# Kernel optimization log

Measured on AMD Instinct MI355X. Metric: run time of the kernel, lower is better.

## Reference

```python
import jax, jax.numpy as jnp
import numpy as np
from jax.ops import segment_sum, segment_max

N_NODES = 100000
N_EDGES = 3200000
F_IN = 512
HIDDEN = 64
N_CLASSES = 16
N_HOPS = 2
LAMBDA_GRAPH = 0.2
LEAKY_ALPHA = 0.2


def setup_inputs() -> dict:
    key = jax.random.key(0)
    ks = jax.random.split(key, 8)
    X = jax.random.normal(ks[0], (N_NODES, F_IN), dtype=jnp.float32)
    W0 = jax.random.normal(ks[1], (F_IN, HIDDEN), dtype=jnp.float32) * (1.0 / np.sqrt(F_IN))
    W1 = jax.random.normal(ks[2], (HIDDEN, N_CLASSES), dtype=jnp.float32) * (1.0 / np.sqrt(HIDDEN))
    a1 = jax.random.normal(ks[3], (N_CLASSES, 1), dtype=jnp.float32)
    a2 = jax.random.normal(ks[4], (N_CLASSES, 1), dtype=jnp.float32)
    W_attn = jax.random.normal(ks[5], (N_NODES, N_CLASSES), dtype=jnp.float32) * 0.1
    gcn_vals = jax.random.uniform(ks[6], (N_EDGES,), dtype=jnp.float32) / 32.0
    edge_index = jax.random.randint(ks[7], (2, N_EDGES), 0, N_NODES, dtype=jnp.int32)
    return {"X": X, "W0": W0, "W1": W1, "a1": a1, "a2": a2,
            "W_attn": W_attn, "gcn_vals": gcn_vals, "edge_index": edge_index}


def _sp_attn_head(Z, src, dst, gcn_vals, a1, a2):
    # per-node scalar scores (GAT-style)
    f1 = (Z @ a1)[:, 0]  # [N]
    f2 = (Z @ a2)[:, 0]  # [N]
    e = jax.nn.leaky_relu(f1[src] + f2[dst], negative_slope=LEAKY_ALPHA)  # [E]
    # sparse softmax over each row (segment by src)
    m = segment_max(e, src, num_segments=N_NODES)
    ex = jnp.exp(e - m[src])
    s = segment_sum(ex, src, num_segments=N_NODES)
    soft = ex / s[src]
    coef = gcn_vals * (1.0 - LAMBDA_GRAPH) + soft * LAMBDA_GRAPH  # [E]
    # sparse_tensor_dense_matmul: out[i] = sum_j coef_ij * Z[j]
    vals = segment_sum(coef[:, None] * Z[dst], src, num_segments=N_NODES)  # [N,C]
    return vals


def reference(X, W0, W1, a1, a2, W_attn, gcn_vals, edge_index):
    src, dst = edge_index[0], edge_index[1]
    # dense MLP layers (inference: keep_prob = 1 => no dropout)
    H = jax.nn.relu(X @ W0)           # [N, HIDDEN]
    Z = H @ W1                        # logits_local [N, C]
    hops = [Z]
    for _ in range(N_HOPS):
        hops.append(_sp_attn_head(hops[-1], src, dst, gcn_vals, a1, a2))
    P = jnp.stack(hops, axis=1)       # [N, K, C]
    # _build_attn: per-node attention over hops
    attn = jnp.einsum('nkc,nc->nk', P, W_attn)
    ceof = jax.nn.softmax(attn, axis=1)
    out = jnp.einsum('nkc,nk->nc', P, ceof)  # [N, C]
    return out
```

## Files before the change

### kernel.cpp

```cpp
#include <hip/hip_runtime.h>
#include <hip/hip_fp16.h>

#define NN 100000
#define NE 3200000
#define FIN 512
#define HIDN 64
#define NC 16
#define LEAKY 0.2f
#define LG 0.2f

#define GM 256
#define HLD2 72
#define MLP_BLKS 391

#define BSH 9
#define NBUCK 196
#define TILE_A 4096
#define SLACK 20480

typedef float4 f4;
typedef short bf16x8 __attribute__((ext_vector_type(8)));
typedef float f32x4 __attribute__((ext_vector_type(4)));
typedef unsigned short ushort_t;

__device__ __forceinline__ bf16x8 cvt8(const f4 a, const f4 b) {
  union { unsigned u[4]; bf16x8 v; } o;
  asm("v_cvt_pk_bf16_f32 %0, %1, %2" : "=v"(o.u[0]) : "v"(a.x), "v"(a.y));
  asm("v_cvt_pk_bf16_f32 %0, %1, %2" : "=v"(o.u[1]) : "v"(a.z), "v"(a.w));
  asm("v_cvt_pk_bf16_f32 %0, %1, %2" : "=v"(o.u[2]) : "v"(b.x), "v"(b.y));
  asm("v_cvt_pk_bf16_f32 %0, %1, %2" : "=v"(o.u[3]) : "v"(b.z), "v"(b.w));
  return o.v;
}

__device__ __forceinline__ float bf16f(ushort_t s) {
  return __uint_as_float(((unsigned)s) << 16);
}
__device__ __forceinline__ ushort_t f2bf(float f) {
  const unsigned u = __float_as_uint(f);
  return (ushort_t)((u + 0x7fffu + ((u >> 16) & 1u)) >> 16);
}
__device__ __forceinline__ int2 ldnt(const int2* p) {
  const int* q = (const int*)p;
  int2 r;
  r.x = __builtin_nontemporal_load(q);
  r.y = __builtin_nontemporal_load(q + 1);
  return r;
}

__global__ __launch_bounds__(256) void k_w0t(const float* __restrict__ W0,
                                             short* __restrict__ W0T,
                                             int* __restrict__ bcnt,
                                             int* __restrict__ gcur) {
  const int i = blockIdx.x*256 + threadIdx.x;
  if (blockIdx.x == 0) {
    bcnt[threadIdx.x] = 0;
    gcur[threadIdx.x] = threadIdx.x * SLACK;
  }
  if (i >= HIDN*FIN) return;
  const int c = i >> 9, k = i & 511;
  W0T[i] = (short)f2bf(W0[(size_t)k*HIDN + c]);
}

__global__ __launch_bounds__(512, 2) void k_mlp3(
    const float* __restrict__ X, const short* __restrict__ W0T,
    const float* __restrict__ W1, const float* __restrict__ a1v,
    const float* __restrict__ a2v, float* __restrict__ Z,
    ushort_t* __restrict__ Zb, float* __restrict__ f1o, float* __restrict__ f2o)
{
  __shared__ __align__(16) char smem[HIDN*FIN*2];
  short* Wb = (short*)smem;
  short (*HsB)[HLD2] = (short(*)[HLD2])smem;
  float* W1s = (float*)(smem + GM*HLD2*2);
  const int t = threadIdx.x;
  const int wid = t >> 6, lane = t & 63;
  const int r = lane & 15, g = lane >> 4;
  const int rowbase = blockIdx.x*GM + wid*32;
  int row0 = rowbase + r;       if (row0 >= NN) row0 = NN-1;
  int row1 = rowbase + 16 + r;  if (row1 >= NN) row1 = NN-1;
  const float* pa0 = X + (size_t)row0*FIN + g*8;
  const float* pa1 = X + (size_t)row1*FIN + g*8;

  f4 xs[4][2][2];
  #pragma unroll
  for (int d=0; d<4; ++d) {
    xs[d][0][0] = *(const f4*)(pa0 + d*32);  xs[d][0][1] = *(const f4*)(pa0 + d*32 + 4);
    xs[d][1][0] = *(const f4*)(pa1 + d*32);  xs[d][1][1] = *(const f4*)(pa1 + d*32 + 4);
  }

  #pragma unroll
  for (int i2 = 0; i2 < 8; ++i2) {
    const int i = t + i2*512;
    const int row = i >> 6;
    const int cb = (i & 63) << 4;
    const bf16x8 v = *(const bf16x8*)(W0T + (size_t)row*FIN + (i & 63)*8);
    *(bf16x8*)((char*)Wb + row*1024 + (cb ^ ((row & 7) << 4))) = v;
  }
  __syncthreads();

  f32x4 acc[2][4];
  #pragma unroll
  for (int m=0;m<2;++m)
    #pragma unroll
    for (int n=0;n<4;++n) acc[m][n] = (f32x4){0.f,0.f,0.f,0.f};

  #pragma unroll
  for (int ks=0; ks<16; ++ks) {
    const int st = ks & 3;
    bf16x8 bh[4];
    #pragma unroll
    for (int n=0;n<4;++n) {
      const int wrow = n*16 + r;
      const int boff = wrow*1024 + ((ks*64 + g*16) ^ ((wrow & 7) << 4));
      bh[n] = *(const bf16x8*)((const char*)Wb + boff);
    }
    const bf16x8 xb0 = cvt8(xs[st][0][0], xs[st][0][1]);
    const bf16x8 xb1 = cvt8(xs[st][1][0], xs[st][1][1]);
    if (ks + 4 < 16) {
      const int ko = (ks+4)*32;
      xs[st][0][0] = *(const f4*)(pa0 + ko);  xs[st][0][1] = *(const f4*)(pa0 + ko + 4);
      xs[st][1][0] = *(const f4*)(pa1 + ko);  xs[st][1][1] = *(const f4*)(pa1 + ko + 4);
    }
    #pragma unroll
    for (int n=0;n<4;++n) {
      acc[0][n] = __builtin_amdgcn_mfma_f32_16x16x32_bf16(xb0, bh[n], acc[0][n], 0,0,0);
      acc[1][n] = __builtin_amdgcn_mfma_f32_16x16x32_bf16(xb1, bh[n], acc[1][n], 0,0,0);
    }
  }
  __syncthreads();

  #pragma unroll
  for (int m=0;m<2;++m) {
    const int hr = wid*32 + m*16 + g*4;
    #pragma unroll
    for (int n=0;n<4;++n)
      #pragma unroll
      for (int q=0;q<4;++q)
        HsB[hr+q][n*16+r] = (short)f2bf(fmaxf(acc[m][n][q], 0.f));
  }
  if (t < 256) *(f4*)(W1s + t*4) = *(const f4*)(W1 + t*4);
  __syncthreads();

  {
    const int en = t >> 1, half = t & 1;
    const int node = blockIdx.x*GM + en;
    if (node < NN) {
      float z[8];
      #pragma unroll
      for (int j=0;j<8;++j) z[j]=0.f;
      const bf16x8* hp = (const bf16x8*)(&HsB[en][0]);
      #pragma unroll
      for (int h8=0; h8<8; ++h8) {
        const bf16x8 hv8 = hp[h8];
        #pragma unroll
        for (int j=0;j<8;++j) {
          const float hv = bf16f((ushort_t)hv8[j]);
          const int h = h8*8 + j;
          const f4 wa = *(const f4*)(W1s + h*NC + half*8);
          const f4 wb = *(const f4*)(W1s + h*NC + half*8 + 4);
          z[0]+=hv*wa.x; z[1]+=hv*wa.y; z[2]+=hv*wa.z; z[3]+=hv*wa.w;
          z[4]+=hv*wb.x; z[5]+=hv*wb.y; z[6]+=hv*wb.z; z[7]+=hv*wb.w;
        }
      }
      f4* zp = (f4*)(Z + (size_t)node*NC + half*8);
      zp[0] = make_float4(z[0],z[1],z[2],z[3]);
      zp[1] = make_float4(z[4],z[5],z[6],z[7]);
      bf16x8 zb;
      #pragma unroll
      for (int j=0;j<8;++j) zb[j] = (short)f2bf(z[j]);
      *(bf16x8*)(Zb + (size_t)node*NC + half*8) = zb;
      float s1=0.f, s2=0.f;
      #pragma unroll
      for (int j=0;j<8;++j) { s1 += z[j]*a1v[half*8+j]; s2 += z[j]*a2v[half*8+j]; }
      s1 += __shfl_xor(s1, 1);
      s2 += __shfl_xor(s2, 1);
      if (half == 0) { f1o[node] = s1; f2o[node] = s2; }
    }
  }
}

__global__ __launch_bounds__(512) void k_binA(const int* __restrict__ src,
    const int* __restrict__ dst, const float* __restrict__ gcn,
    int* __restrict__ bcnt, int* __restrict__ gcur, int2* __restrict__ tmp)
{
  __shared__ int cnt[256];
  __shared__ int scn[256];
  __shared__ int cur[256];
  __shared__ int gbase[256];
  __shared__ int2 stage[TILE_A];
  __shared__ unsigned char sb[TILE_A];
  const int t = threadIdx.x;
  const int e0 = blockIdx.x*TILE_A;
  const int ecount = min(TILE_A, NE - e0);
  if (t < 256) cnt[t] = 0;
  __syncthreads();
  int w0v[8], w1v[8], bv[8];
  #pragma unroll
  for (int it=0; it<8; ++it) {
    const int i = e0 + it*512 + t;
    bv[it] = -1;
    if (i < NE) {
      const int s_ = src[i];
      const int b = s_ >> BSH;
      bv[it] = b;
      w0v[it] = dst[i] | ((s_ & ((1<<BSH)-1)) << 17);
      w1v[it] = __float_as_int(gcn[i]);
      atomicAdd(&cnt[b], 1);
    }
  }
  __syncthreads();
  if (t < 256) scn[t] = cnt[t];
  __syncthreads();
  for (int off=1; off<256; off<<=1) {
    const int x = (t>=off && t<256) ? scn[t-off] : 0;
    __syncthreads();
    if (t < 256) scn[t] += x;
    __syncthreads();
  }
  if (t < 256) {
    cur[t] = scn[t] - cnt[t];
    if (cnt[t] > 0) {
      gbase[t] = atomicAdd(&gcur[t], cnt[t]);
      atomicAdd(&bcnt[t], cnt[t]);
    }
  }
  __syncthreads();
  #pragma unroll
  for (int it=0; it<8; ++it) {
    if (bv[it] >= 0) {
      const int pos = atomicAdd(&cur[bv[it]], 1);
      stage[pos] = make_int2(w0v[it], w1v[it]);
      sb[pos] = (unsigned char)bv[it];
    }
  }
  __syncthreads();
  #pragma unroll
  for (int it=0; it<8; ++it) {
    const int slot = it*512 + t;
    if (slot < ecount) {
      const int b = sb[slot];
      const int gd = gbase[b] + slot - (scn[b] - cnt[b]);
      tmp[gd] = stage[slot];
    }
  }
}

__global__ __launch_bounds__(512) void k_binB(const int* __restrict__ bcnt,
    const int2* __restrict__ tmp, int* __restrict__ rowptr, int2* __restrict__ cvp)
{
  __shared__ int cnt[512];
  __shared__ int scn[512];
  __shared__ int cur[512];
  __shared__ int bs[256];
  __shared__ int baseSh;
  const int t = threadIdx.x;
  const int b = blockIdx.x;
  const int node0 = b << BSH;
  const int n = bcnt[b];
  const int2* tsl = tmp + (size_t)b*SLACK;
  if (t < 256) bs[t] = (t < NBUCK) ? bcnt[t] : 0;
  cnt[t] = 0;
  __syncthreads();
  for (int off=1; off<256; off<<=1) {
    const int x = (t>=off && t<256) ? bs[t-off] : 0;
    __syncthreads();
    if (t < 256) bs[t] += x;
    __syncthreads();
  }
  if (t == 0) baseSh = bs[b] - n;
  __syncthreads();
  const int base = baseSh;
  for (int i = t; i < n; i += 512)
    atomicAdd(&cnt[tsl[i].x >> 17], 1);
  __syncthreads();
  scn[t] = cnt[t];
  __syncthreads();
  for (int off=1; off<512; off<<=1) {
    const int x = (t>=off) ? scn[t-off] : 0;
    __syncthreads();
    scn[t] += x;
    __syncthreads();
  }
  const int excl = scn[t] - cnt[t];
  cur[t] = excl;
  if (node0 + t < NN) rowptr[node0 + t] = base + excl;
  if (b == 0 && t == 0) rowptr[NN] = NE;
  __syncthreads();
  for (int i = t; i < n; i += 512) {
    const int2 e = tsl[i];
    const int ls = e.x >> 17;
    const int p = base + atomicAdd(&cur[ls], 1);
    cvp[p] = make_int2(e.x & 0x1FFFF, e.y);
  }
}

__global__ __launch_bounds__(256) void k_hop(const int* __restrict__ rowptr,
    const int2* __restrict__ cvp,
    const ushort_t* __restrict__ Zb, const float* __restrict__ f1in,
    const float* __restrict__ f2in, ushort_t* __restrict__ Zoutb,
    float* __restrict__ f1out, float* __restrict__ f2out,
    const float* __restrict__ a1v, const float* __restrict__ a2v)
{
  __shared__ __align__(16) int2 rowbuf[8][64];
  const int t = threadIdx.x;
  const int lane = t & 31;
  const int hw = t >> 5;
  const int row = blockIdx.x*8 + hw;
  if (row >= NN) return;
  const int start = rowptr[row], end = rowptr[row+1];
  const int deg = end - start;
  const int c = lane & 15, g = (lane >> 4) & 1;

  if (deg == 0) {
    if (g == 0) {
      Zoutb[(size_t)row*NC + c] = 0;
      if (c == 0) { f1out[row] = 0.f; f2out[row] = 0.f; }
    }
    return;
  }
  const float f1r = f1in[row];

  if (deg <= 64) {
    int cc0 = 0, cc1 = 0; float vv0 = 0.f, vv1 = 0.f;
    float e0 = -1e30f, e1 = -1e30f;
    if (lane < deg) {
      const int2 p = ldnt(&cvp[start + lane]);
      cc0 = p.x; vv0 = __int_as_float(p.y);
      const float x = f1r + f2in[cc0];
      e0 = (x > 0.f) ? x : LEAKY*x;
    }
    if (32 + lane < deg) {
      const int2 p = ldnt(&cvp[start + 32 + lane]);
      cc1 = p.x; vv1 = __int_as_float(p.y);
      const float x = f1r + f2in[cc1];
      e1 = (x > 0.f) ? x : LEAKY*x;
    }
    float m = fmaxf(e0, e1);
    #pragma unroll
    for (int msk=1; msk<32; msk<<=1) m = fmaxf(m, __shfl_xor(m, msk));
    const float ex0 = (lane < deg) ? __expf(e0 - m) : 0.f;
    const float ex1 = (32 + lane < deg) ? __expf(e1 - m) : 0.f;
    float s = ex0 + ex1;
    #pragma unroll
    for (int msk=1; msk<32; msk<<=1) s += __shfl_xor(s, msk);
    const float lgs = LG / s;
    const int npass = (deg + 3) >> 2;
    if (lane < deg)
      rowbuf[hw][lane] = make_int2(cc0, __float_as_int((1.f-LG)*vv0 + ex0*lgs));
    if (32 + lane < deg)
      rowbuf[hw][32 + lane] = make_int2(cc1, __float_as_int((1.f-LG)*vv1 + ex1*lgs));
    for (int z = deg + lane; z < 4*npass; z += 32) rowbuf[hw][z] = make_int2(0, 0);
    asm volatile("s_waitcnt lgkmcnt(0)" ::: "memory");
    float accv = 0.f;
    for (int p0 = 0; p0 < npass; p0 += 8) {
      int4 pr[8]; ushort_t u0[8], u1[8];
      #pragma unroll
      for (int j=0;j<8;++j) {
        if (p0 + j < npass)
          pr[j] = *(const int4*)(&rowbuf[hw][(p0+j)*4 + g*2]);
        else
          pr[j] = make_int4(0, 0, 0, 0);
      }
      #pragma unroll
      for (int j=0;j<8;++j) {
        u0[j] = Zb[(size_t)pr[j].x*NC + c];
        u1[j] = Zb[(size_t)pr[j].z*NC + c];
      }
      #pragma unroll
      for (int j=0;j<8;++j) {
        accv += __int_as_float(pr[j].y) * bf16f(u0[j]);
        accv += __int_as_float(pr[j].w) * bf16f(u1[j]);
      }
    }
    accv += __shfl_xor(accv, 16);
    if (g == 0) {
      Zoutb[(size_t)row*NC + c] = f2bf(accv);
      float s1 = accv * a1v[c];
      float s2 = accv * a2v[c];
      #pragma unroll
      for (int msk=1; msk<16; msk<<=1) { s1 += __shfl_xor(s1, msk); s2 += __shfl_xor(s2, msk); }
      if (c == 0) { f1out[row] = s1; f2out[row] = s2; }
    }
  } else {
    const int nit = (deg + 31) >> 5;
    float m = -1e30f;
    for (int it=0; it<nit; ++it) {
      const int idx = start + it*32 + lane;
      if (idx < end) {
        const int2 p = ldnt(&cvp[idx]);
        const float x = f1r + f2in[p.x];
        m = fmaxf(m, (x>0.f)?x:LEAKY*x);
      }
    }
    #pragma unroll
    for (int msk=1; msk<32; msk<<=1) m = fmaxf(m, __shfl_xor(m, msk));
    float s = 0.f;
    for (int it=0; it<nit; ++it) {
      const int idx = start + it*32 + lane;
      if (idx < end) {
        const int2 p = ldnt(&cvp[idx]);
        const float x = f1r + f2in[p.x];
        s += __expf(((x>0.f)?x:LEAKY*x) - m);
      }
    }
    #pragma unroll
    for (int msk=1; msk<32; msk<<=1) s += __shfl_xor(s, msk);
    const float lgs = LG / s;
    float a[16];
    #pragma unroll
    for (int k=0;k<16;++k) a[k]=0.f;
    for (int it=0; it<nit; ++it) {
      const int idx = start + it*32 + lane;
      if (idx < end) {
        const int2 p = ldnt(&cvp[idx]);
        const float x = f1r + f2in[p.x];
        const float coef = (1.f-LG)*__int_as_float(p.y) + __expf(((x>0.f)?x:LEAKY*x) - m)*lgs;
        const ushort_t* zp = Zb + (size_t)p.x*NC;
        #pragma unroll
        for (int k=0;k<16;++k) a[k] += coef * bf16f(zp[k]);
      }
    }
    #pragma unroll
    for (int msk=1; msk<32; msk<<=1) {
      #pragma unroll
      for (int k=0;k<16;++k) a[k] += __shfl_xor(a[k], msk);
    }
    if (lane == 0) {
      #pragma unroll
      for (int k=0;k<16;++k) Zoutb[(size_t)row*NC + k] = f2bf(a[k]);
      float s1=0.f, s2=0.f;
      #pragma unroll
      for (int k=0;k<16;++k) { s1 += a[k]*a1v[k]; s2 += a[k]*a2v[k]; }
      f1out[row]=s1; f2out[row]=s2;
    }
  }
}

__global__ __launch_bounds__(256) void k_hop2mix(const int* __restrict__ rowptr,
    const int2* __restrict__ cvp,
    const ushort_t* __restrict__ Z1b, const float* __restrict__ f1in,
    const float* __restrict__ f2in, const float* __restrict__ Z0,
    const float* __restrict__ Wat, float* __restrict__ outp)
{
  __shared__ __align__(16) int2 rowbuf[8][64];
  const int t = threadIdx.x;
  const int lane = t & 31;
  const int hw = t >> 5;
  const int row = blockIdx.x*8 + hw;
  if (row >= NN) return;
  const int start = rowptr[row], end = rowptr[row+1];
  const int deg = end - start;
  const int c = lane & 15, g = (lane >> 4) & 1;

  if (deg > 64) {
    const float f1r = f1in[row];
    const int nit = (deg + 31) >> 5;
    float m = -1e30f;
    for (int it=0; it<nit; ++it) {
      const int idx = start + it*32 + lane;
      if (idx < end) {
        const float x = f1r + f2in[ldnt(&cvp[idx]).x];
        m = fmaxf(m, (x>0.f)?x:LEAKY*x);
      }
    }
    #pragma unroll
    for (int msk=1; msk<32; msk<<=1) m = fmaxf(m, __shfl_xor(m, msk));
    float s = 0.f;
    for (int it=0; it<nit; ++it) {
      const int idx = start + it*32 + lane;
      if (idx < end) {
        const float x = f1r + f2in[ldnt(&cvp[idx]).x];
        s += __expf(((x>0.f)?x:LEAKY*x) - m);
      }
    }
    #pragma unroll
    for (int msk=1; msk<32; msk<<=1) s += __shfl_xor(s, msk);
    const float lgs = LG / s;
    float a[16];
    #pragma unroll
    for (int k=0;k<16;++k) a[k]=0.f;
    for (int it=0; it<nit; ++it) {
      const int idx = start + it*32 + lane;
      if (idx < end) {
        const int2 p = ldnt(&cvp[idx]);
        const float x = f1r + f2in[p.x];
        const float coef = (1.f-LG)*__int_as_float(p.y) + __expf(((x>0.f)?x:LEAKY*x) - m)*lgs;
        const ushort_t* zp = Z1b + (size_t)p.x*NC;
        #pragma unroll
        for (int k=0;k<16;++k) a[k] += coef * bf16f(zp[k]);
      }
    }
    #pragma unroll
    for (int msk=1; msk<32; msk<<=1) {
      #pragma unroll
      for (int k=0;k<16;++k) a[k] += __shfl_xor(a[k], msk);
    }
    if (lane == 0) {
      float t0=0.f, t1=0.f, t2=0.f;
      for (int k=0;k<16;++k) {
        const float w = Wat[(size_t)row*NC + k];
        t0 += Z0[(size_t)row*NC + k]*w;
        t1 += bf16f(Z1b[(size_t)row*NC + k])*w;
        t2 += a[k]*w;
      }
      const float mm = fmaxf(t0, fmaxf(t1, t2));
      const float q0 = __expf(t0-mm), q1 = __expf(t1-mm), q2 = __expf(t2-mm);
      const float inv = 1.f/(q0+q1+q2);
      for (int k=0;k<16;++k)
        outp[(size_t)row*NC + k] =
          (q0*Z0[(size_t)row*NC + k] + q1*bf16f(Z1b[(size_t)row*NC + k]) + q2*a[k])*inv;
    }
    return;
  }

  float accv = 0.f;
  if (deg > 0) {
    const float f1r = f1in[row];
    int cc0 = 0, cc1 = 0; float vv0 = 0.f, vv1 = 0.f;
    float e0 = -1e30f, e1 = -1e30f;
    if (lane < deg) {
      const int2 p = ldnt(&cvp[start + lane]);
      cc0 = p.x; vv0 = __int_as_float(p.y);
      const float x = f1r + f2in[cc0];
      e0 = (x > 0.f) ? x : LEAKY*x;
    }
    if (32 + lane < deg) {
      const int2 p = ldnt(&cvp[start + 32 + lane]);
      cc1 = p.x; vv1 = __int_as_float(p.y);
      const float x = f1r + f2in[cc1];
      e1 = (x > 0.f) ? x : LEAKY*x;
    }
    float m = fmaxf(e0, e1);
    #pragma unroll
    for (int msk=1; msk<32; msk<<=1) m = fmaxf(m, __shfl_xor(m, msk));
    const float ex0 = (lane < deg) ? __expf(e0 - m) : 0.f;
    const float ex1 = (32 + lane < deg) ? __expf(e1 - m) : 0.f;
    float s = ex0 + ex1;
    #pragma unroll
    for (int msk=1; msk<32; msk<<=1) s += __shfl_xor(s, msk);
    const float lgs = LG / s;
    const int npass = (deg + 3) >> 2;
    if (lane < deg)
      rowbuf[hw][lane] = make_int2(cc0, __float_as_int((1.f-LG)*vv0 + ex0*lgs));
    if (32 + lane < deg)
      rowbuf[hw][32 + lane] = make_int2(cc1, __float_as_int((1.f-LG)*vv1 + ex1*lgs));
    for (int z = deg + lane; z < 4*npass; z += 32) rowbuf[hw][z] = make_int2(0, 0);
    asm volatile("s_waitcnt lgkmcnt(0)" ::: "memory");
    for (int p0 = 0; p0 < npass; p0 += 8) {
      int4 pr[8]; ushort_t u0[8], u1[8];
      #pragma unroll
      for (int j=0;j<8;++j) {
        if (p0 + j < npass)
          pr[j] = *(const int4*)(&rowbuf[hw][(p0+j)*4 + g*2]);
        else
          pr[j] = make_int4(0, 0, 0, 0);
      }
      #pragma unroll
      for (int j=0;j<8;++j) {
        u0[j] = Z1b[(size_t)pr[j].x*NC + c];
        u1[j] = Z1b[(size_t)pr[j].z*NC + c];
      }
      #pragma unroll
      for (int j=0;j<8;++j) {
        accv += __int_as_float(pr[j].y) * bf16f(u0[j]);
        accv += __int_as_float(pr[j].w) * bf16f(u1[j]);
      }
    }
    accv += __shfl_xor(accv, 16);
  }
  if (g == 0) {
    const float z0v = Z0[(size_t)row*NC + c];
    const float z1v = bf16f(Z1b[(size_t)row*NC + c]);
    const float wv  = Wat[(size_t)row*NC + c];
    float t0 = z0v*wv, t1 = z1v*wv, t2 = accv*wv;
    #pragma unroll
    for (int msk=1; msk<16; msk<<=1) {
      t0 += __shfl_xor(t0, msk); t1 += __shfl_xor(t1, msk); t2 += __shfl_xor(t2, msk);
    }
    const float mm = fmaxf(t0, fmaxf(t1, t2));
    const float q0 = __expf(t0-mm), q1 = __expf(t1-mm), q2 = __expf(t2-mm);
    const float inv = 1.f/(q0+q1+q2);
    outp[(size_t)row*NC + c] = (q0*z0v + q1*z1v + q2*accv)*inv;
  }
}

extern "C" void kernel_launch(void* const* d_in, const int* in_sizes, int n_in,
                              void* d_out, int out_size, void* d_ws, size_t ws_size,
                              hipStream_t stream) {
  const float* X   = (const float*)d_in[0];
  const float* W0  = (const float*)d_in[1];
  const float* W1  = (const float*)d_in[2];
  const float* a1  = (const float*)d_in[3];
  const float* a2  = (const float*)d_in[4];
  const float* Wat = (const float*)d_in[5];
  const float* gcn = (const float*)d_in[6];
  const int*   ei  = (const int*)d_in[7];
  const int* src = ei;
  const int* dst = ei + NE;
  float* out = (float*)d_out;

  float* Z0      = (float*)d_ws;
  ushort_t* Z0b  = (ushort_t*)(Z0 + (size_t)NN*NC);
  ushort_t* Z1b  = Z0b + (size_t)NN*NC;
  float* fA1  = (float*)(Z1b + (size_t)NN*NC);
  float* fA2  = fA1 + NN;
  float* fB1  = fA2 + NN;
  float* fB2  = fB1 + NN;
  int* rowptr = (int*)(fB2 + NN);
  int* bcnt   = rowptr + (NN + 4);
  int* gcur   = bcnt + 256;
  short* W0T  = (short*)(gcur + 256);
  int2* cvp   = (int2*)(W0T + HIDN*FIN);
  int2* tmp   = cvp + NE;

  k_w0t<<<(HIDN*FIN + 255)/256, 256, 0, stream>>>(W0, W0T, bcnt, gcur);
  k_mlp3<<<MLP_BLKS, 512, 0, stream>>>(X, W0T, W1, a1, a2, Z0, Z0b, fA1, fA2);
  k_binA<<<(NE + TILE_A - 1)/TILE_A, 512, 0, stream>>>(src, dst, gcn, bcnt, gcur, tmp);
  k_binB<<<NBUCK, 512, 0, stream>>>(bcnt, tmp, rowptr, cvp);
  k_hop<<<12500, 256, 0, stream>>>(rowptr, cvp, Z0b, fA1, fA2, Z1b, fB1, fB2, a1, a2);
  k_hop2mix<<<12500, 256, 0, stream>>>(rowptr, cvp, Z1b, fB1, fB2, Z0, Wat, out);
}
```

Measured before the change: 227.2 us.

## Merge MLP and edge-binning kernels into one launch via block specialization

Folds the dense MLP kernel and the first edge-binning pass into a single kernel. Block indices below the MLP count run the GEMM, and the remaining blocks bin edges into src buckets, sharing one shared-memory buffer. The aim is to let the compute-heavy MLP and the memory/atomic-heavy binning run on the GPU at the same time, and to remove one launch and the serialization between them. In exchange, the binning blocks now take the MLP kernel's larger shared-memory footprint and its launch bounds, which could limit their occupancy.

Result: faster. 205.9 us (median of 3 runs) (-9.4%).

```diff
diff --git a/kernel.cpp b/kernel.cpp
--- a/kernel.cpp
+++ b/kernel.cpp
@@ -16,6 +16,7 @@
 #define BSH 9
 #define NBUCK 196
 #define TILE_A 4096
+#define NBINA 782
 #define SLACK 20480
 
 typedef float4 f4;
@@ -61,185 +62,186 @@
   W0T[i] = (short)f2bf(W0[(size_t)k*HIDN + c]);
 }
 
-__global__ __launch_bounds__(512, 2) void k_mlp3(
+__global__ __launch_bounds__(512, 2) void k_mlpA(
     const float* __restrict__ X, const short* __restrict__ W0T,
     const float* __restrict__ W1, const float* __restrict__ a1v,
     const float* __restrict__ a2v, float* __restrict__ Z,
-    ushort_t* __restrict__ Zb, float* __restrict__ f1o, float* __restrict__ f2o)
+    ushort_t* __restrict__ Zb, float* __restrict__ f1o, float* __restrict__ f2o,
+    const int* __restrict__ src, const int* __restrict__ dst,
+    const float* __restrict__ gcn, int* __restrict__ bcnt,
+    int* __restrict__ gcur, int2* __restrict__ tmp)
 {
   __shared__ __align__(16) char smem[HIDN*FIN*2];
-  short* Wb = (short*)smem;
-  short (*HsB)[HLD2] = (short(*)[HLD2])smem;
-  float* W1s = (float*)(smem + GM*HLD2*2);
   const int t = threadIdx.x;
-  const int wid = t >> 6, lane = t & 63;
-  const int r = lane & 15, g = lane >> 4;
-  const int rowbase = blockIdx.x*GM + wid*32;
-  int row0 = rowbase + r;       if (row0 >= NN) row0 = NN-1;
-  int row1 = rowbase + 16 + r;  if (row1 >= NN) row1 = NN-1;
-  const float* pa0 = X + (size_t)row0*FIN + g*8;
-  const float* pa1 = X + (size_t)row1*FIN + g*8;
-
-  f4 xs[4][2][2];
-  #pragma unroll
-  for (int d=0; d<4; ++d) {
-    xs[d][0][0] = *(const f4*)(pa0 + d*32);  xs[d][0][1] = *(const f4*)(pa0 + d*32 + 4);
-    xs[d][1][0] = *(const f4*)(pa1 + d*32);  xs[d][1][1] = *(const f4*)(pa1 + d*32 + 4);
-  }
-
-  #pragma unroll
-  for (int i2 = 0; i2 < 8; ++i2) {
-    const int i = t + i2*512;
-    const int row = i >> 6;
-    const int cb = (i & 63) << 4;
-    const bf16x8 v = *(const bf16x8*)(W0T + (size_t)row*FIN + (i & 63)*8);
-    *(bf16x8*)((char*)Wb + row*1024 + (cb ^ ((row & 7) << 4))) = v;
-  }
-  __syncthreads();
-
-  f32x4 acc[2][4];
-  #pragma unroll
-  for (int m=0;m<2;++m)
-    #pragma unroll
-    for (int n=0;n<4;++n) acc[m][n] = (f32x4){0.f,0.f,0.f,0.f};
-
-  #pragma unroll
-  for (int ks=0; ks<16; ++ks) {
-    const int st = ks & 3;
-    bf16x8 bh[4];
-    #pragma unroll
-    for (int n=0;n<4;++n) {
-      const int wrow = n*16 + r;
-      const int boff = wrow*1024 + ((ks*64 + g*16) ^ ((wrow & 7) << 4));
-      bh[n] = *(const bf16x8*)((const char*)Wb + boff);
-    }
-    const bf16x8 xb0 = cvt8(xs[st][0][0], xs[st][0][1]);
-    const bf16x8 xb1 = cvt8(xs[st][1][0], xs[st][1][1]);
-    if (ks + 4 < 16) {
-      const int ko = (ks+4)*32;
-      xs[st][0][0] = *(const f4*)(pa0 + ko);  xs[st][0][1] = *(const f4*)(pa0 + ko + 4);
-      xs[st][1][0] = *(const f4*)(pa1 + ko);  xs[st][1][1] = *(const f4*)(pa1 + ko + 4);
-    }
-    #pragma unroll
-    for (int n=0;n<4;++n) {
-      acc[0][n] = __builtin_amdgcn_mfma_f32_16x16x32_bf16(xb0, bh[n], acc[0][n], 0,0,0);
-      acc[1][n] = __builtin_amdgcn_mfma_f32_16x16x32_bf16(xb1, bh[n], acc[1][n], 0,0,0);
-    }
-  }
-  __syncthreads();
-
-  #pragma unroll
-  for (int m=0;m<2;++m) {
-    const int hr = wid*32 + m*16 + g*4;
-    #pragma unroll
-    for (int n=0;n<4;++n)
-      #pragma unroll
-      for (int q=0;q<4;++q)
-        HsB[hr+q][n*16+r] = (short)f2bf(fmaxf(acc[m][n][q], 0.f));
-  }
-  if (t < 256) *(f4*)(W1s + t*4) = *(const f4*)(W1 + t*4);
-  __syncthreads();
-
-  {
-    const int en = t >> 1, half = t & 1;
-    const int node = blockIdx.x*GM + en;
-    if (node < NN) {
-      float z[8];
-      #pragma unroll
-      for (int j=0;j<8;++j) z[j]=0.f;
-      const bf16x8* hp = (const bf16x8*)(&HsB[en][0]);
-      #pragma unroll
-      for (int h8=0; h8<8; ++h8) {
-        const bf16x8 hv8 = hp[h8];
+
+  if (blockIdx.x < MLP_BLKS) {
+    short* Wb = (short*)smem;
+    short (*HsB)[HLD2] = (short(*)[HLD2])smem;
+    float* W1s = (float*)(smem + GM*HLD2*2);
+    const int wid = t >> 6, lane = t & 63;
+    const int r = lane & 15, g = lane >> 4;
+    const int rowbase = blockIdx.x*GM + wid*32;
+    int row0 = rowbase + r;       if (row0 >= NN) row0 = NN-1;
+    int row1 = rowbase + 16 + r;  if (row1 >= NN) row1 = NN-1;
+    const float* pa0 = X + (size_t)row0*FIN + g*8;
+    const float* pa1 = X + (size_t)row1*FIN + g*8;
+
+    f4 xs[4][2][2];
+    #pragma unroll
+    for (int d=0; d<4; ++d) {
+      xs[d][0][0] = *(const f4*)(pa0 + d*32);  xs[d][0][1] = *(const f4*)(pa0 + d*32 + 4);
+      xs[d][1][0] = *(const f4*)(pa1 + d*32);  xs[d][1][1] = *(const f4*)(pa1 + d*32 + 4);
+    }
+
+    #pragma unroll
+    for (int i2 = 0; i2 < 8; ++i2) {
+      const int i = t + i2*512;
+      const int row = i >> 6;
+      const int cb = (i & 63) << 4;
+      const bf16x8 v = *(const bf16x8*)(W0T + (size_t)row*FIN + (i & 63)*8);
+      *(bf16x8*)((char*)Wb + row*1024 + (cb ^ ((row & 7) << 4))) = v;
+    }
+    __syncthreads();
+
+    f32x4 acc[2][4];
+    #pragma unroll
+    for (int m=0;m<2;++m)
+      #pragma unroll
+      for (int n=0;n<4;++n) acc[m][n] = (f32x4){0.f,0.f,0.f,0.f};
+
+    #pragma unroll
+    for (int ks=0; ks<16; ++ks) {
+      const int st = ks & 3;
+      bf16x8 bh[4];
+      #pragma unroll
+      for (int n=0;n<4;++n) {
+        const int wrow = n*16 + r;
+        const int boff = wrow*1024 + ((ks*64 + g*16) ^ ((wrow & 7) << 4));
+        bh[n] = *(const bf16x8*)((const char*)Wb + boff);
+      }
+      const bf16x8 xb0 = cvt8(xs[st][0][0], xs[st][0][1]);
+      const bf16x8 xb1 = cvt8(xs[st][1][0], xs[st][1][1]);
+      if (ks + 4 < 16) {
+        const int ko = (ks+4)*32;
+        xs[st][0][0] = *(const f4*)(pa0 + ko);  xs[st][0][1] = *(const f4*)(pa0 + ko + 4);
+        xs[st][1][0] = *(const f4*)(pa1 + ko);  xs[st][1][1] = *(const f4*)(pa1 + ko + 4);
+      }
+      #pragma unroll
+      for (int n=0;n<4;++n) {
+        acc[0][n] = __builtin_amdgcn_mfma_f32_16x16x32_bf16(xb0, bh[n], acc[0][n], 0,0,0);
+        acc[1][n] = __builtin_amdgcn_mfma_f32_16x16x32_bf16(xb1, bh[n], acc[1][n], 0,0,0);
+      }
+    }
+    __syncthreads();
+
+    #pragma unroll
+    for (int m=0;m<2;++m) {
+      const int hr = wid*32 + m*16 + g*4;
+      #pragma unroll
+      for (int n=0;n<4;++n)
         #pragma unroll
-        for (int j=0;j<8;++j) {
-          const float hv = bf16f((ushort_t)hv8[j]);
-          const int h = h8*8 + j;
-          const f4 wa = *(const f4*)(W1s + h*NC + half*8);
-          const f4 wb = *(const f4*)(W1s + h*NC + half*8 + 4);
-          z[0]+=hv*wa.x; z[1]+=hv*wa.y; z[2]+=hv*wa.z; z[3]+=hv*wa.w;
-          z[4]+=hv*wb.x; z[5]+=hv*wb.y; z[6]+=hv*wb.z; z[7]+=hv*wb.w;
+        for (int q=0;q<4;++q)
+          HsB[hr+q][n*16+r] = (short)f2bf(fmaxf(acc[m][n][q], 0.f));
+    }
+    if (t < 256) *(f4*)(W1s + t*4) = *(const f4*)(W1 + t*4);
+    __syncthreads();
+
+    {
+      const int en = t >> 1, half = t & 1;
+      const int node = blockIdx.x*GM + en;
+      if (node < NN) {
+        float z[8];
+        #pragma unroll
+        for (int j=0;j<8;++j) z[j]=0.f;
+        const bf16x8* hp = (const bf16x8*)(&HsB[en][0]);
+        #pragma unroll
+        for (int h8=0; h8<8; ++h8) {
+          const bf16x8 hv8 = hp[h8];
+          #pragma unroll
+          for (int j=0;j<8;++j) {
+            const float hv = bf16f((ushort_t)hv8[j]);
+            const int h = h8*8 + j;
+            const f4 wa = *(const f4*)(W1s + h*NC + half*8);
+            const f4 wb = *(const f4*)(W1s + h*NC + half*8 + 4);
+            z[0]+=hv*wa.x; z[1]+=hv*wa.y; z[2]+=hv*wa.z; z[3]+=hv*wa.w;
+            z[4]+=hv*wb.x; z[5]+=hv*wb.y; z[6]+=hv*wb.z; z[7]+=hv*wb.w;
+          }
         }
-      }
-      f4* zp = (f4*)(Z + (size_t)node*NC + half*8);
-      zp[0] = make_float4(z[0],z[1],z[2],z[3]);
-      zp[1] = make_float4(z[4],z[5],z[6],z[7]);
-      bf16x8 zb;
-      #pragma unroll
-      for (int j=0;j<8;++j) zb[j] = (short)f2bf(z[j]);
-      *(bf16x8*)(Zb + (size_t)node*NC + half*8) = zb;
-      float s1=0.f, s2=0.f;
-      #pragma unroll
-      for (int j=0;j<8;++j) { s1 += z[j]*a1v[half*8+j]; s2 += z[j]*a2v[half*8+j]; }
-      s1 += __shfl_xor(s1, 1);
-      s2 += __shfl_xor(s2, 1);
-      if (half == 0) { f1o[node] = s1; f2o[node] = s2; }
-    }
-  }
-}
-
-__global__ __launch_bounds__(512) void k_binA(const int* __restrict__ src,
-    const int* __restrict__ dst, const float* __restrict__ gcn,
-    int* __restrict__ bcnt, int* __restrict__ gcur, int2* __restrict__ tmp)
-{
-  __shared__ int cnt[256];
-  __shared__ int scn[256];
-  __shared__ int cur[256];
-  __shared__ int gbase[256];
-  __shared__ int2 stage[TILE_A];
-  __shared__ unsigned char sb[TILE_A];
-  const int t = threadIdx.x;
-  const int e0 = blockIdx.x*TILE_A;
-  const int ecount = min(TILE_A, NE - e0);
-  if (t < 256) cnt[t] = 0;
-  __syncthreads();
-  int w0v[8], w1v[8], bv[8];
-  #pragma unroll
-  for (int it=0; it<8; ++it) {
-    const int i = e0 + it*512 + t;
-    bv[it] = -1;
-    if (i < NE) {
-      const int s_ = src[i];
-      const int b = s_ >> BSH;
-      bv[it] = b;
-      w0v[it] = dst[i] | ((s_ & ((1<<BSH)-1)) << 17);
-      w1v[it] = __float_as_int(gcn[i]);
-      atomicAdd(&cnt[b], 1);
-    }
-  }
-  __syncthreads();
-  if (t < 256) scn[t] = cnt[t];
-  __syncthreads();
-  for (int off=1; off<256; off<<=1) {
-    const int x = (t>=off && t<256) ? scn[t-off] : 0;
-    __syncthreads();
-    if (t < 256) scn[t] += x;
-    __syncthreads();
-  }
-  if (t < 256) {
-    cur[t] = scn[t] - cnt[t];
-    if (cnt[t] > 0) {
-      gbase[t] = atomicAdd(&gcur[t], cnt[t]);
-      atomicAdd(&bcnt[t], cnt[t]);
-    }
-  }
-  __syncthreads();
-  #pragma unroll
-  for (int it=0; it<8; ++it) {
-    if (bv[it] >= 0) {
-      const int pos = atomicAdd(&cur[bv[it]], 1);
-      stage[pos] = make_int2(w0v[it], w1v[it]);
-      sb[pos] = (unsigned char)bv[it];
-    }
-  }
-  __syncthreads();
-  #pragma unroll
-  for (int it=0; it<8; ++it) {
-    const int slot = it*512 + t;
-    if (slot < ecount) {
-      const int b = sb[slot];
-      const int gd = gbase[b] + slot - (scn[b] - cnt[b]);
-      tmp[gd] = stage[slot];
+        f4* zp = (f4*)(Z + (size_t)node*NC + half*8);
+        zp[0] = make_float4(z[0],z[1],z[2],z[3]);
+        zp[1] = make_float4(z[4],z[5],z[6],z[7]);
+        bf16x8 zb;
+        #pragma unroll
+        for (int j=0;j<8;++j) zb[j] = (short)f2bf(z[j]);
+        *(bf16x8*)(Zb + (size_t)node*NC + half*8) = zb;
+        float s1=0.f, s2=0.f;
+        #pragma unroll
+        for (int j=0;j<8;++j) { s1 += z[j]*a1v[half*8+j]; s2 += z[j]*a2v[half*8+j]; }
+        s1 += __shfl_xor(s1, 1);
+        s2 += __shfl_xor(s2, 1);
+        if (half == 0) { f1o[node] = s1; f2o[node] = s2; }
+      }
+    }
+  } else {
+    int* cnt  = (int*)smem;
+    int* scn  = cnt + 256;
+    int* cur  = scn + 256;
+    int* gbase= cur + 256;
+    int2* stage = (int2*)(gbase + 256);
+    unsigned char* sb = (unsigned char*)(stage + TILE_A);
+    const int blk = blockIdx.x - MLP_BLKS;
+    const int e0 = blk*TILE_A;
+    const int ecount = min(TILE_A, NE - e0);
+    if (t < 256) cnt[t] = 0;
+    __syncthreads();
+    int w0v[8], w1v[8], bv[8];
+    #pragma unroll
+    for (int it=0; it<8; ++it) {
+      const int i = e0 + it*512 + t;
+      bv[it] = -1;
+      if (i < NE) {
+        const int s_ = src[i];
+        const int b = s_ >> BSH;
+        bv[it] = b;
+        w0v[it] = dst[i] | ((s_ & ((1<<BSH)-1)) << 17);
+        w1v[it] = __float_as_int(gcn[i]);
+        atomicAdd(&cnt[b], 1);
+      }
+    }
+    __syncthreads();
+    if (t < 256) scn[t] = cnt[t];
+    __syncthreads();
+    for (int off=1; off<256; off<<=1) {
+      const int x = (t>=off && t<256) ? scn[t-off] : 0;
+      __syncthreads();
+      if (t < 256) scn[t] += x;
+      __syncthreads();
+    }
+    if (t < 256) {
+      cur[t] = scn[t] - cnt[t];
+      if (cnt[t] > 0) {
+        gbase[t] = atomicAdd(&gcur[t], cnt[t]);
+        atomicAdd(&bcnt[t], cnt[t]);
+      }
+    }
+    __syncthreads();
+    #pragma unroll
+    for (int it=0; it<8; ++it) {
+      if (bv[it] >= 0) {
+        const int pos = atomicAdd(&cur[bv[it]], 1);
+        stage[pos] = make_int2(w0v[it], w1v[it]);
+        sb[pos] = (unsigned char)bv[it];
+      }
+    }
+    __syncthreads();
+    #pragma unroll
+    for (int it=0; it<8; ++it) {
+      const int slot = it*512 + t;
+      if (slot < ecount) {
+        const int b = sb[slot];
+        const int gd = gbase[b] + slot - (scn[b] - cnt[b]);
+        tmp[gd] = stage[slot];
+      }
     }
   }
 }
@@ -613,8 +615,8 @@
   int2* tmp   = cvp + NE;
 
   k_w0t<<<(HIDN*FIN + 255)/256, 256, 0, stream>>>(W0, W0T, bcnt, gcur);
-  k_mlp3<<<MLP_BLKS, 512, 0, stream>>>(X, W0T, W1, a1, a2, Z0, Z0b, fA1, fA2);
-  k_binA<<<(NE + TILE_A - 1)/TILE_A, 512, 0, stream>>>(src, dst, gcn, bcnt, gcur, tmp);
+  k_mlpA<<<MLP_BLKS + NBINA, 512, 0, stream>>>(X, W0T, W1, a1, a2, Z0, Z0b, fA1, fA2,
+                                               src, dst, gcn, bcnt, gcur, tmp);
   k_binB<<<NBUCK, 512, 0, stream>>>(bcnt, tmp, rowptr, cvp);
   k_hop<<<12500, 256, 0, stream>>>(rowptr, cvp, Z0b, fA1, fA2, Z1b, fB1, fB2, a1, a2);
   k_hop2mix<<<12500, 256, 0, stream>>>(rowptr, cvp, Z1b, fB1, fB2, Z0, Wat, out);
```
